# Performance work log

Hardware: AMD Instinct MI355X
Metric: run time of the kernel (lower is better)

## Reference

```python
import jax, jax.numpy as jnp
import numpy as np

B, S, V, D, H, F, GH, NC, L = 64, 256, 50000, 1024, 16, 4096, 100, 7, 4
DH = D // H


def _ln(x, g, b):
    m = x.mean(-1, keepdims=True)
    v = x.var(-1, keepdims=True)
    return (x - m) / jnp.sqrt(v + 1e-5) * g + b


def setup_inputs() -> dict:
    key = jax.random.key(0)
    ks = iter(jax.random.split(key, 40))
    nrm = lambda shp, s=0.02: jax.random.normal(next(ks), shp, jnp.float32) * s
    inp = {}
    inp["src"] = jax.random.randint(next(ks), (B, S), 0, V)
    inp["em_seq"] = jax.random.normal(next(ks), (B, S, 7), jnp.float32)
    inp["d_ids"] = jax.random.randint(next(ks), (B, 1), 0, B)
    inp["ut_len"] = jax.random.randint(next(ks), (B,), 1, S + 1)
    inp["emb"] = jax.random.uniform(next(ks), (V, D), jnp.float32, -0.1, 0.1)
    inp["Wqkv"] = nrm((L, 3 * D, D)); inp["bqkv"] = jnp.zeros((L, 3 * D), jnp.float32)
    inp["Wo"] = nrm((L, D, D)); inp["bo"] = jnp.zeros((L, D), jnp.float32)
    inp["W1"] = nrm((L, F, D)); inp["b1"] = jnp.zeros((L, F), jnp.float32)
    inp["W2"] = nrm((L, D, F)); inp["b2"] = jnp.zeros((L, D), jnp.float32)
    inp["ln1_g"] = jnp.ones((L, D), jnp.float32); inp["ln1_b"] = jnp.zeros((L, D), jnp.float32)
    inp["ln2_g"] = jnp.ones((L, D), jnp.float32); inp["ln2_b"] = jnp.zeros((L, D), jnp.float32)
    inp["gru_Wih"] = nrm((3 * GH, 7), 0.1); inp["gru_Whh"] = nrm((3 * GH, GH), 0.1)
    inp["gru_bih"] = jnp.zeros((3 * GH,), jnp.float32); inp["gru_bhh"] = jnp.zeros((3 * GH,), jnp.float32)
    inp["dec_W"] = jax.random.uniform(next(ks), (NC, 2 * D + GH), jnp.float32, -0.1, 0.1)
    inp["dec_b"] = jnp.zeros((NC,), jnp.float32)
    return inp


def reference(src, em_seq, d_ids, ut_len, emb, Wqkv, bqkv, Wo, bo, W1, b1, W2, b2,
              ln1_g, ln1_b, ln2_g, ln2_b, gru_Wih, gru_Whh, gru_bih, gru_bhh,
              dec_W, dec_b):
    # embedding + scale + sinusoidal positional encoding
    x = emb[src] * jnp.sqrt(jnp.float32(D))                      # [B,S,D]
    pos = jnp.arange(S, dtype=jnp.float32)[:, None]
    div = jnp.exp(jnp.arange(0, D, 2, dtype=jnp.float32) * (-jnp.log(10000.0) / D))
    pe = jnp.stack([jnp.sin(pos * div), jnp.cos(pos * div)], -1).reshape(S, D)
    x = x + pe

    causal = jnp.tril(jnp.ones((S, S), bool))
    neg = jnp.finfo(x.dtype).min
    for l in range(L):  # post-norm transformer encoder layers (PyTorch default)
        qkv = x @ Wqkv[l].T + bqkv[l]
        q, k, v = jnp.split(qkv, 3, -1)
        q = q.reshape(B, S, H, DH); k = k.reshape(B, S, H, DH); v = v.reshape(B, S, H, DH)
        sc = jnp.einsum('bqhd,bkhd->bhqk', q, k) / jnp.sqrt(jnp.float32(DH))
        sc = jnp.where(causal, sc, neg)
        a = jax.nn.softmax(sc, -1)
        o = jnp.einsum('bhqk,bkhd->bqhd', a, v).reshape(B, S, D)
        x = _ln(x + o @ Wo[l].T + bo[l], ln1_g[l], ln1_b[l])
        ff = jax.nn.relu(x @ W1[l].T + b1[l]) @ W2[l].T + b2[l]
        x = _ln(x + ff, ln2_g[l], ln2_b[l])

    # emotion GRU (PyTorch GRU equations), scan over time
    xp = jnp.einsum('bsf,gf->sbg', em_seq, gru_Wih) + gru_bih    # [S,B,3*GH]

    def step(h, xt):
        hp = h @ gru_Whh.T + gru_bhh
        xr, xz, xn = jnp.split(xt, 3, -1)
        hr, hz, hn = jnp.split(hp, 3, -1)
        r = jax.nn.sigmoid(xr + hr)
        z = jax.nn.sigmoid(xz + hz)
        n = jnp.tanh(xn + r * hn)
        h = (1.0 - z) * n + z * h
        return h, h

    _, hs = jax.lax.scan(step, jnp.zeros((B, GH), x.dtype), xp)
    emo = hs.transpose(1, 0, 2)                                  # [B,S,GH]

    # ragged gather of the 'main' utterance per dialogue + broadcast-concat
    lens = ut_len[d_ids[:, 0]]                                   # [B]
    main = x[jnp.arange(B), lens - 1]                            # [B,D]
    pair = jnp.concatenate([x, jnp.broadcast_to(main[:, None, :], (B, S, D))], -1)
    valid = (jnp.arange(S)[None, :] < lens[:, None])[..., None]
    pair = jnp.where(valid, pair, 0.0)                           # zeros beyond ut_len, as in torch loop
    dec_ip = jnp.concatenate([pair, emo], -1)                    # [B,S,2D+GH]
    return dec_ip @ dec_W.T + dec_b                              # [B,S,NC]
```

## Files before the change

kernel.cpp:

```cpp
#include <hip/hip_runtime.h>
#include <hip/hip_bf16.h>
#include <math.h>

#define BB 64
#define SS 256
#define DD 1024
#define HH 16
#define FFN 4096
#define GHH 100
#define NCC 7
#define LL 4
#define TT (BB*SS)
#define DHH 64

typedef unsigned short u16;
typedef unsigned int u32;
typedef __attribute__((ext_vector_type(4))) float f32x4;
typedef __attribute__((ext_vector_type(8))) short s16x8;
typedef __attribute__((ext_vector_type(4))) unsigned short u16x4;

__device__ __forceinline__ u16 f2bf(float f) {
  union { float f; u32 u; } x; x.f = f;
  u32 r = x.u + 0x7FFFu + ((x.u >> 16) & 1u);
  return (u16)(r >> 16);
}
__device__ __forceinline__ float bf2f(u16 b) {
  union { u32 u; float f; } x; x.u = ((u32)b) << 16;
  return x.f;
}

__global__ void k_f2bf4(const float* __restrict__ s0, u16* __restrict__ d0, int n0,
                        const float* __restrict__ s1, u16* __restrict__ d1, int n1,
                        const float* __restrict__ s2, u16* __restrict__ d2, int n2,
                        const float* __restrict__ s3, u16* __restrict__ d3, int n3) {
  int stride = gridDim.x * blockDim.x;
  int total = n0 + n1 + n2 + n3;
  for (int i = blockIdx.x * blockDim.x + threadIdx.x; i < total; i += stride) {
    const float* s; u16* d; int j = i;
    if (j < n0) { s = s0; d = d0; }
    else {
      j -= n0;
      if (j < n1) { s = s1; d = d1; }
      else {
        j -= n1;
        if (j < n2) { s = s2; d = d2; }
        else { j -= n2; s = s3; d = d3; }
      }
    }
    f32x4 v = *(const f32x4*)(s + (size_t)j * 4);
    u16x4 o;
    o[0] = f2bf(v[0]); o[1] = f2bf(v[1]); o[2] = f2bf(v[2]); o[3] = f2bf(v[3]);
    *(u16x4*)(d + (size_t)j * 4) = o;
  }
}

__global__ void k_pe(float* __restrict__ pe) {
  int i = blockIdx.x * blockDim.x + threadIdx.x;
  if (i >= SS * DD / 2) return;
  int s = i / (DD / 2), j = i % (DD / 2);
  float div = __expf((float)(2 * j) * (-9.210340371976184f / (float)DD));
  float a = (float)s * div;
  pe[s * DD + 2 * j]     = sinf(a);
  pe[s * DD + 2 * j + 1] = cosf(a);
}

__global__ void k_embed(const int* __restrict__ src, const float* __restrict__ emb,
                        const float* __restrict__ pe, u16* __restrict__ xb) {
  int i = blockIdx.x * blockDim.x + threadIdx.x;
  if (i >= TT * DD / 4) return;
  int t = i / (DD / 4);
  int d4 = (i % (DD / 4)) * 4;
  int s = t % SS;
  int tok = src[t];
  f32x4 e = *(const f32x4*)(emb + (size_t)tok * DD + d4);
  f32x4 p = *(const f32x4*)(pe + (size_t)s * DD + d4);
  u16x4 o;
  o[0] = f2bf(e[0] * 32.0f + p[0]); o[1] = f2bf(e[1] * 32.0f + p[1]);
  o[2] = f2bf(e[2] * 32.0f + p[2]); o[3] = f2bf(e[3] * 32.0f + p[3]);
  *(u16x4*)(xb + (size_t)t * DD + d4) = o;
}

#define MEMF asm volatile("" ::: "memory")
#define GBAR do { MEMF; __builtin_amdgcn_sched_barrier(0); __builtin_amdgcn_s_barrier(); __builtin_amdgcn_sched_barrier(0); MEMF; } while(0)
#define VMW4 asm volatile("s_waitcnt vmcnt(4)" ::: "memory")

#define STG(P, isB, h, l, buf, kt) \
  __builtin_amdgcn_global_load_lds( \
    (const __attribute__((address_space(1))) u32*)(P[h][l] + (kt)), \
    (__attribute__((address_space(3))) u32*)(smem + (buf)*65536 + (isB)*32768 + (h)*16384 + (l)*8192 + wid*1024), \
    16, 0, 0)

#define LDB(buf) do { \
  _Pragma("unroll") for (int nf = 0; nf < 4; nf++) \
  _Pragma("unroll") for (int kk = 0; kk < 2; kk++) { \
    int rel = (wn*64 + nf*16 + lm)*128 + kk*64 + lg*16; \
    bq[nf][kk] = *(const s16x8*)(smem + (buf)*65536 + 32768 + (rel ^ (((rel>>9)&1)<<5))); \
  } } while(0)

#define LDA(buf, q) do { \
  _Pragma("unroll") for (int ml = 0; ml < 2; ml++) \
  _Pragma("unroll") for (int kk = 0; kk < 2; kk++) { \
    int rel = (wm*128 + ((q)*2+ml)*16 + lm)*128 + kk*64 + lg*16; \
    aq[ml][kk] = *(const s16x8*)(smem + (buf)*65536 + (rel ^ (((rel>>9)&1)<<5))); \
  } } while(0)

#define MFMAQ(q) do { \
  __builtin_amdgcn_s_setprio(1); \
  _Pragma("unroll") for (int ml = 0; ml < 2; ml++) \
  _Pragma("unroll") for (int nf = 0; nf < 4; nf++) \
  _Pragma("unroll") for (int kk = 0; kk < 2; kk++) \
    acc[(q)*2+ml][nf] = __builtin_amdgcn_mfma_f32_16x16x32_bf16(aq[ml][kk], bq[nf][kk], acc[(q)*2+ml][nf], 0, 0, 0); \
  __builtin_amdgcn_s_setprio(0); \
} while(0)

template<int EPI>
__global__ __launch_bounds__(512, 2)
void k_gemm256(const u16* __restrict__ A, const u16* __restrict__ W,
               const float* __restrict__ bias, u16* __restrict__ C,
               int M, int N, int K) {
  extern __shared__ char smem[];
  const int tid = threadIdx.x;
  const int lane = tid & 63;
  const int wid = tid >> 6;
  const int lm = lane & 15, lg = lane >> 4;
  const int wm = wid >> 2, wn = wid & 3;

  const int NB = N >> 8;
  const int nwg = gridDim.x;
  const int bid = blockIdx.x;
  const int cpx = nwg >> 3;
  const int swzb = (bid & 7) * cpx + (bid >> 3);
  const int m0 = (swzb / NB) << 8;
  const int n0 = (swzb % NB) << 8;

  const u16* pA[2][2];
  const u16* pB[2][2];
#pragma unroll
  for (int h = 0; h < 2; h++)
#pragma unroll
    for (int l = 0; l < 2; l++) {
      int rel = h * 16384 + l * 8192 + tid * 16;
      int sb = rel ^ (((rel >> 9) & 1) << 5);
      int grow = sb >> 7;
      int gcol = (sb & 127) >> 1;
      pA[h][l] = A + (size_t)(m0 + grow) * K + gcol;
      pB[h][l] = W + (size_t)(n0 + grow) * K + gcol;
    }

  f32x4 acc[8][4];
#pragma unroll
  for (int i = 0; i < 8; i++)
#pragma unroll
    for (int j = 0; j < 4; j++) acc[i][j] = (f32x4){0.f, 0.f, 0.f, 0.f};

  s16x8 bq[4][2];
  s16x8 aq[2][2];

  const int NT = K >> 6;

  STG(pB,1,0,0,0,0); STG(pB,1,0,1,0,0); STG(pB,1,1,0,0,0); STG(pB,1,1,1,0,0);
  STG(pA,0,0,0,0,0); STG(pA,0,0,1,0,0); STG(pA,0,1,0,0,0); STG(pA,0,1,1,0,0);
  STG(pB,1,0,0,1,64); STG(pB,1,0,1,1,64); STG(pB,1,1,0,1,64); STG(pB,1,1,1,1,64);
  VMW4;
  GBAR;

  for (int i = 0; i < (NT >> 1); i++) {
    const int t1k = (2*i + 1) * 64;
    int t2 = 2*i + 2; if (t2 >= NT) t2 -= NT;
    int t3 = 2*i + 3; if (t3 >= NT) t3 -= NT;
    const int t2k = t2 * 64, t3k = t3 * 64;

    LDB(0); LDA(0,0);
    STG(pA,0,0,0,1,t1k); STG(pA,0,0,1,1,t1k);
    GBAR; MFMAQ(0); GBAR;
    LDA(0,1);
    STG(pA,0,1,0,1,t1k); STG(pA,0,1,1,1,t1k);
    STG(pB,1,0,0,0,t2k); STG(pB,1,0,1,0,t2k);
    GBAR; MFMAQ(1); GBAR;
    LDA(0,2);
    STG(pB,1,1,0,0,t2k); STG(pB,1,1,1,0,t2k);
    GBAR; MFMAQ(2); GBAR;
    LDA(0,3);
    GBAR; MFMAQ(3); VMW4; GBAR;
    LDB(1); LDA(1,0);
    STG(pA,0,0,0,0,t2k); STG(pA,0,0,1,0,t2k);
    GBAR; MFMAQ(0); GBAR;
    LDA(1,1);
    STG(pA,0,1,0,0,t2k); STG(pA,0,1,1,0,t2k);
    GBAR; MFMAQ(1); GBAR;
    LDA(1,2);
    STG(pB,1,0,0,1,t3k); STG(pB,1,0,1,1,t3k);
    GBAR; MFMAQ(2); GBAR;
    LDA(1,3);
    STG(pB,1,1,0,1,t3k); STG(pB,1,1,1,1,t3k);
    GBAR; MFMAQ(3); VMW4; GBAR;
  }

  float bn[4];
#pragma unroll
  for (int nf = 0; nf < 4; nf++) bn[nf] = bias[n0 + wn*64 + nf*16 + lm];
#pragma unroll
  for (int mf = 0; mf < 8; mf++)
#pragma unroll
    for (int nf = 0; nf < 4; nf++) {
      int col = n0 + wn*64 + nf*16 + lm;
#pragma unroll
      for (int r = 0; r < 4; r++) {
        int row = m0 + wm*128 + mf*16 + lg*4 + r;
        float v = acc[mf][nf][r] + bn[nf];
        if (EPI == 1) v = fmaxf(v, 0.f);
        C[(size_t)row * N + col] = f2bf(v);
      }
    }
}

__global__ __launch_bounds__(256, 2)
void k_attn(const u16* __restrict__ qkv, u16* __restrict__ o) {
  const int h = blockIdx.x;
  const int b = blockIdx.y;
  const int lane = threadIdx.x & 63;
  const int w = threadIdx.x >> 6;
  const int lm = lane & 15, lg = lane >> 4;

  __shared__ u16 Ks[64 * 64];
  __shared__ u16 Vt[64 * 64];
  __shared__ u16 Ps[4][64 * 64];

  const size_t tokbase = (size_t)b * SS;

  s16x8 aq[4][2];
#pragma unroll
  for (int mf = 0; mf < 4; mf++) {
    const u16* qrow = qkv + (tokbase + w * 64 + mf * 16 + lm) * 3072 + h * 64;
#pragma unroll
    for (int kk = 0; kk < 2; kk++)
      aq[mf][kk] = *(const s16x8*)(qrow + kk * 32 + lg * 8);
  }

  f32x4 zero = {0.f, 0.f, 0.f, 0.f};
  f32x4 oacc[4][4];
#pragma unroll
  for (int mf = 0; mf < 4; mf++)
#pragma unroll
    for (int df = 0; df < 4; df++) oacc[mf][df] = zero;
  float m_run[16], l_run[16];
#pragma unroll
  for (int r = 0; r < 16; r++) { m_run[r] = -3e38f; l_run[r] = 0.f; }

  for (int kb = 0; kb < 4; kb++) {
    __syncthreads();
    {
      int krow = threadIdx.x >> 2;
      int seg  = (threadIdx.x & 3) * 16;
      const u16* ksrc = qkv + (tokbase + kb * 64 + krow) * 3072 + 1024 + h * 64 + seg;
      s16x8 v0 = *(const s16x8*)(ksrc);
      s16x8 v1 = *(const s16x8*)(ksrc + 8);
      *(s16x8*)&Ks[krow * 64 + seg] = v0;
      *(s16x8*)&Ks[krow * 64 + seg + 8] = v1;
      const u16* vsrc = qkv + (tokbase + kb * 64 + krow) * 3072 + 2048 + h * 64 + seg;
      s16x8 w0 = *(const s16x8*)(vsrc);
      s16x8 w1 = *(const s16x8*)(vsrc + 8);
#pragma unroll
      for (int e = 0; e < 8; e++) {
        Vt[(seg + e) * 64 + krow]     = (u16)w0[e];
        Vt[(seg + 8 + e) * 64 + krow] = (u16)w1[e];
      }
    }
    __syncthreads();
    if (w < kb) continue;

    s16x8 bk[4][2];
#pragma unroll
    for (int nf = 0; nf < 4; nf++)
#pragma unroll
      for (int kk = 0; kk < 2; kk++)
        bk[nf][kk] = *(const s16x8*)&Ks[(nf * 16 + lm) * 64 + kk * 32 + lg * 8];

    const int colbase = kb * 64;
#pragma unroll
    for (int mf = 0; mf < 4; mf++) {
      f32x4 sfr[4];
#pragma unroll
      for (int nf = 0; nf < 4; nf++) {
        f32x4 acc = zero;
#pragma unroll
        for (int kk = 0; kk < 2; kk++)
          acc = __builtin_amdgcn_mfma_f32_16x16x32_bf16(aq[mf][kk], bk[nf][kk], acc, 0, 0, 0);
        sfr[nf] = acc;
      }
      const int rowbase = w * 64 + mf * 16 + lg * 4;
#pragma unroll
      for (int nf = 0; nf < 4; nf++) {
        int col = colbase + nf * 16 + lm;
#pragma unroll
        for (int r = 0; r < 4; r++) {
          float v = sfr[nf][r] * 0.125f;
          sfr[nf][r] = (col <= rowbase + r) ? v : -1e30f;
        }
      }
#pragma unroll
      for (int r = 0; r < 4; r++) {
        float m = fmaxf(fmaxf(sfr[0][r], sfr[1][r]), fmaxf(sfr[2][r], sfr[3][r]));
#pragma unroll
        for (int off = 1; off < 16; off <<= 1) m = fmaxf(m, __shfl_xor(m, off));
        int idx = mf * 4 + r;
        float mnew = fmaxf(m_run[idx], m);
        float fo = __expf(m_run[idx] - mnew);
        m_run[idx] = mnew;
        float ps = 0.f;
#pragma unroll
        for (int nf = 0; nf < 4; nf++) {
          float p = __expf(sfr[nf][r] - mnew);
          sfr[nf][r] = p;
          ps += p;
        }
#pragma unroll
        for (int off = 1; off < 16; off <<= 1) ps += __shfl_xor(ps, off);
        l_run[idx] = l_run[idx] * fo + ps;
#pragma unroll
        for (int df = 0; df < 4; df++) oacc[mf][df][r] *= fo;
      }
#pragma unroll
      for (int nf = 0; nf < 4; nf++)
#pragma unroll
        for (int r = 0; r < 4; r++)
          Ps[w][(mf * 16 + lg * 4 + r) * 64 + nf * 16 + lm] = f2bf(sfr[nf][r]);
    }
    asm volatile("" ::: "memory");
    s16x8 bv[4][2];
#pragma unroll
    for (int df = 0; df < 4; df++)
#pragma unroll
      for (int kk = 0; kk < 2; kk++)
        bv[df][kk] = *(const s16x8*)&Vt[(df * 16 + lm) * 64 + kk * 32 + lg * 8];
#pragma unroll
    for (int mf = 0; mf < 4; mf++) {
      s16x8 pa[2];
#pragma unroll
      for (int kk = 0; kk < 2; kk++)
        pa[kk] = *(const s16x8*)&Ps[w][(mf * 16 + lm) * 64 + kk * 32 + lg * 8];
#pragma unroll
      for (int df = 0; df < 4; df++)
#pragma unroll
        for (int kk = 0; kk < 2; kk++)
          oacc[mf][df] = __builtin_amdgcn_mfma_f32_16x16x32_bf16(pa[kk], bv[df][kk], oacc[mf][df], 0, 0, 0);
    }
  }

#pragma unroll
  for (int mf = 0; mf < 4; mf++)
#pragma unroll
    for (int df = 0; df < 4; df++)
#pragma unroll
      for (int r = 0; r < 4; r++) {
        int row = w * 64 + mf * 16 + lg * 4 + r;
        float val = oacc[mf][df][r] / l_run[mf * 4 + r];
        o[(tokbase + row) * 1024 + h * 64 + df * 16 + lm] = f2bf(val);
      }
}

__global__ __launch_bounds__(256)
void k_ln(u16* __restrict__ xb, const u16* __restrict__ tmp,
          const float* __restrict__ gam, const float* __restrict__ bet) {
  int t = blockIdx.x;
  int tid = threadIdx.x;
  u16x4 a4 = *(const u16x4*)(xb + (size_t)t * DD + tid * 4);
  u16x4 u4 = *(const u16x4*)(tmp + (size_t)t * DD + tid * 4);
  f32x4 v;
#pragma unroll
  for (int e = 0; e < 4; e++) v[e] = bf2f(a4[e]) + bf2f(u4[e]);
  float s = v[0] + v[1] + v[2] + v[3];
  float s2 = v[0]*v[0] + v[1]*v[1] + v[2]*v[2] + v[3]*v[3];
#pragma unroll
  for (int off = 32; off >= 1; off >>= 1) {
    s  += __shfl_xor(s, off);
    s2 += __shfl_xor(s2, off);
  }
  __shared__ float red[8];
  int w = tid >> 6;
  if ((tid & 63) == 0) { red[w] = s; red[4 + w] = s2; }
  __syncthreads();
  s  = red[0] + red[1] + red[2] + red[3];
  s2 = red[4] + red[5] + red[6] + red[7];
  float mean = s * (1.f / 1024.f);
  float var = s2 * (1.f / 1024.f) - mean * mean;
  float rstd = rsqrtf(var + 1e-5f);
  f32x4 g4 = *(const f32x4*)(gam + tid * 4);
  f32x4 b4 = *(const f32x4*)(bet + tid * 4);
  u16x4 yo;
#pragma unroll
  for (int e = 0; e < 4; e++)
    yo[e] = f2bf((v[e] - mean) * rstd * g4[e] + b4[e]);
  *(u16x4*)(xb + (size_t)t * DD + tid * 4) = yo;
}

#define QL(X) X(0) X(1) X(2) X(3) X(4) X(5) X(6) X(7) X(8) X(9) X(10) X(11)
#define F7(X) X(0) X(1) X(2) X(3) X(4) X(5) X(6)

__global__ __launch_bounds__(256, 1)
void k_gru(const float* __restrict__ em, const float* __restrict__ Wih,
           const float* __restrict__ bih, const float* __restrict__ Whh,
           const float* __restrict__ bhh, float* __restrict__ emo) {
  const int b = blockIdx.x;
  const int tid = threadIdx.x;
  const int iraw = tid >> 1;
  const int i = iraw < 100 ? iraw : 99;
  const bool act = iraw < 100;
  const int half = tid & 1;
  __shared__ __align__(16) float h[2][104];

  const float* rowR = Whh + (size_t)i * 100 + half * 50;
  const float* rowZ = Whh + (size_t)(100 + i) * 100 + half * 50;
  const float* rowN = Whh + (size_t)(200 + i) * 100 + half * 50;

#define LOADQ(q) \
  f32x4 wr##q = {rowR[4*q], rowR[4*q+1], rowR[4*q+2], rowR[4*q+3]}; \
  f32x4 wz##q = {rowZ[4*q], rowZ[4*q+1], rowZ[4*q+2], rowZ[4*q+3]}; \
  f32x4 wn##q = {rowN[4*q], rowN[4*q+1], rowN[4*q+2], rowN[4*q+3]};
  QL(LOADQ)
#undef LOADQ
  f32x4 wr12 = {rowR[48], rowR[49], 0.f, 0.f};
  f32x4 wz12 = {rowZ[48], rowZ[49], 0.f, 0.f};
  f32x4 wn12 = {rowN[48], rowN[49], 0.f, 0.f};

#define LOADI(f) \
  float wir##f = Wih[i * 7 + f]; \
  float wiz##f = Wih[(100 + i) * 7 + f]; \
  float win##f = Wih[(200 + i) * 7 + f];
  F7(LOADI)
#undef LOADI
  const float br = bhh[i], bz = bhh[100 + i], bn = bhh[200 + i];
  const float xbr = bih[i], xbz = bih[100 + i], xbn = bih[200 + i];

  if (tid < 104) { h[0][tid] = 0.f; h[1][tid] = 0.f; }
  __syncthreads();

  const float* eb = em + (size_t)b * SS * 7;
#define DECLE(f) float e##f = eb[f];
  F7(DECLE)
#undef DECLE

  for (int s = 0; s < SS; ++s) {
    const int cur = s & 1, nxt = cur ^ 1;
    float sr = xbr, sz = xbz, sn = xbn;
#define MACI(f) sr += wir##f * e##f; sz += wiz##f * e##f; sn += win##f * e##f;
    F7(MACI)
#undef MACI
    {
      int sp = (s + 1 < SS) ? s + 1 : s;
#define LDE(f) e##f = eb[sp * 7 + f];
      F7(LDE)
#undef LDE
    }
    const float* hb = &h[cur][half * 52];
    f32x4 ar4 = {0.f,0.f,0.f,0.f}, az4 = {0.f,0.f,0.f,0.f}, an4 = {0.f,0.f,0.f,0.f};
#define MACQ(q) { f32x4 hv = *(const f32x4*)(hb + 4*q); \
    ar4 += wr##q * hv; az4 += wz##q * hv; an4 += wn##q * hv; }
    QL(MACQ) MACQ(12)
#undef MACQ
    float ar = (ar4[0] + ar4[1]) + (ar4[2] + ar4[3]);
    float az = (az4[0] + az4[1]) + (az4[2] + az4[3]);
    float an = (an4[0] + an4[1]) + (an4[2] + an4[3]);
    ar += __shfl_xor(ar, 1);
    az += __shfl_xor(az, 1);
    an += __shfl_xor(an, 1);
    if (act && half == 0) {
      int slot = i + (i >= 50 ? 2 : 0);
      float hold = h[cur][slot];
      float rr = 1.f / (1.f + __expf(-(sr + ar + br)));
      float zz = 1.f / (1.f + __expf(-(sz + az + bz)));
      float nx = sn + rr * (an + bn);
      float e2 = __expf(-2.f * fabsf(nx));
      float th = (1.f - e2) / (1.f + e2);
      float nn = copysignf(th, nx);
      float hn = (1.f - zz) * nn + zz * hold;
      h[nxt][slot] = hn;
      emo[((size_t)b * SS + s) * GHH + i] = hn;
    }
    __syncthreads();
  }
}

__global__ void k_main(const int* __restrict__ d_ids, const int* __restrict__ ut_len,
                       const u16* __restrict__ x, const float* __restrict__ decW,
                       float* __restrict__ md) {
  int b = blockIdx.x;
  int lane = threadIdx.x;
  int len = ut_len[d_ids[b]];
  const u16* xr = x + ((size_t)b * SS + (len - 1)) * DD;
  float acc[NCC];
#pragma unroll
  for (int c = 0; c < NCC; c++) acc[c] = 0.f;
  for (int d = lane; d < DD; d += 64) {
    float xv = bf2f(xr[d]);
#pragma unroll
    for (int c = 0; c < NCC; c++) acc[c] += xv * decW[(size_t)c * 2148 + 1024 + d];
  }
#pragma unroll
  for (int c = 0; c < NCC; c++) {
#pragma unroll
    for (int off = 32; off >= 1; off >>= 1) acc[c] += __shfl_xor(acc[c], off);
  }
  if (lane == 0) {
#pragma unroll
    for (int c = 0; c < NCC; c++) md[b * NCC + c] = acc[c];
  }
}

__global__ __launch_bounds__(256)
void k_dec(const u16* __restrict__ x, const float* __restrict__ emo,
           const float* __restrict__ md, const float* __restrict__ decW,
           const float* __restrict__ decb, const int* __restrict__ d_ids,
           const int* __restrict__ ut_len, float* __restrict__ out) {
  int grp = threadIdx.x >> 6, lane = threadIdx.x & 63;
  int t = blockIdx.x * 4 + grp;
  int b = t / SS, s = t % SS;
  int len = ut_len[d_ids[b]];
  bool valid = s < len;
  float acc[NCC];
#pragma unroll
  for (int c = 0; c < NCC; c++) acc[c] = 0.f;
  if (valid) {
    const u16* xrow = x + (size_t)t * DD;
    for (int d = lane; d < DD; d += 64) {
      float xv = bf2f(xrow[d]);
#pragma unroll
      for (int c = 0; c < NCC; c++) acc[c] += xv * decW[(size_t)c * 2148 + d];
    }
  }
  {
    const float* er = emo + (size_t)t * GHH;
    for (int d = lane; d < GHH; d += 64) {
      float ev = er[d];
#pragma unroll
      for (int c = 0; c < NCC; c++) acc[c] += ev * decW[(size_t)c * 2148 + 2048 + d];
    }
  }
#pragma unroll
  for (int c = 0; c < NCC; c++) {
#pragma unroll
    for (int off = 32; off >= 1; off >>= 1) acc[c] += __shfl_xor(acc[c], off);
  }
  if (lane == 0) {
#pragma unroll
    for (int c = 0; c < NCC; c++) {
      float v = acc[c] + (valid ? md[b * NCC + c] : 0.f) + decb[c];
      out[(size_t)t * NCC + c] = v;
    }
  }
}

extern "C" void kernel_launch(void* const* d_in, const int* in_sizes, int n_in,
                              void* d_out, int out_size, void* d_ws, size_t ws_size,
                              hipStream_t stream) {
  const int*   src    = (const int*)d_in[0];
  const float* em_seq = (const float*)d_in[1];
  const int*   d_ids  = (const int*)d_in[2];
  const int*   ut_len = (const int*)d_in[3];
  const float* emb    = (const float*)d_in[4];
  const float* Wqkv   = (const float*)d_in[5];
  const float* bqkv   = (const float*)d_in[6];
  const float* Wo     = (const float*)d_in[7];
  const float* bo     = (const float*)d_in[8];
  const float* W1     = (const float*)d_in[9];
  const float* b1     = (const float*)d_in[10];
  const float* W2     = (const float*)d_in[11];
  const float* b2     = (const float*)d_in[12];
  const float* ln1g   = (const float*)d_in[13];
  const float* ln1b   = (const float*)d_in[14];
  const float* ln2g   = (const float*)d_in[15];
  const float* ln2b   = (const float*)d_in[16];
  const float* gWih   = (const float*)d_in[17];
  const float* gWhh   = (const float*)d_in[18];
  const float* gbih   = (const float*)d_in[19];
  const float* gbhh   = (const float*)d_in[20];
  const float* decW   = (const float*)d_in[21];
  const float* decb   = (const float*)d_in[22];
  float* out = (float*)d_out;

  char* wsp = (char*)d_ws;
  auto take = [&](size_t n) { char* p = wsp; wsp += (n + 255) & ~(size_t)255; return p; };

  u16*   wqkvb = (u16*)take((size_t)3072 * 1024 * 2);
  u16*   wob   = (u16*)take((size_t)1024 * 1024 * 2);
  u16*   w1b   = (u16*)take((size_t)4096 * 1024 * 2);
  u16*   w2b   = (u16*)take((size_t)1024 * 4096 * 2);
  float* pe    = (float*)take((size_t)SS * DD * 4);
  u16*   xb    = (u16*)take((size_t)TT * DD * 2);
  u16*   big   = (u16*)take((size_t)TT * FFN * 2);
  u16*   ob    = (u16*)take((size_t)TT * DD * 2);
  u16*   tmp16 = (u16*)take((size_t)TT * DD * 2);
  float* emo   = (float*)take((size_t)BB * SS * GHH * 4);
  float* md    = (float*)take((size_t)BB * NCC * 4);

  (void)hipFuncSetAttribute((const void*)&k_gemm256<0>,
      hipFuncAttributeMaxDynamicSharedMemorySize, 131072);
  (void)hipFuncSetAttribute((const void*)&k_gemm256<1>,
      hipFuncAttributeMaxDynamicSharedMemorySize, 131072);

  k_gru<<<BB, 256, 0, stream>>>(em_seq, gWih, gbih, gWhh, gbhh, emo);

  k_pe<<<(SS * DD / 2 + 255) / 256, 256, 0, stream>>>(pe);
  k_embed<<<TT * DD / 4 / 256, 256, 0, stream>>>(src, emb, pe, xb);

  for (int l = 0; l < LL; ++l) {
    k_f2bf4<<<2048, 256, 0, stream>>>(
        Wqkv + (size_t)l * 3072 * 1024, wqkvb, 3072 * 1024 / 4,
        Wo   + (size_t)l * 1024 * 1024, wob,   1024 * 1024 / 4,
        W1   + (size_t)l * 4096 * 1024, w1b,   4096 * 1024 / 4,
        W2   + (size_t)l * 1024 * 4096, w2b,   1024 * 4096 / 4);

    k_gemm256<0><<<(TT/256) * (3072/256), 512, 131072, stream>>>(
        xb, wqkvb, bqkv + (size_t)l * 3072, big, TT, 3072, 1024);
    k_attn<<<dim3(HH, BB), 256, 0, stream>>>(big, ob);
    k_gemm256<0><<<(TT/256) * (1024/256), 512, 131072, stream>>>(
        ob, wob, bo + (size_t)l * 1024, tmp16, TT, 1024, 1024);
    k_ln<<<TT, 256, 0, stream>>>(xb, tmp16, ln1g + (size_t)l * DD, ln1b + (size_t)l * DD);
    k_gemm256<1><<<(TT/256) * (4096/256), 512, 131072, stream>>>(
        xb, w1b, b1 + (size_t)l * 4096, big, TT, 4096, 1024);
    k_gemm256<0><<<(TT/256) * (1024/256), 512, 131072, stream>>>(
        big, w2b, b2 + (size_t)l * 1024, tmp16, TT, 1024, 4096);
    k_ln<<<TT, 256, 0, stream>>>(xb, tmp16, ln2g + (size_t)l * DD, ln2b + (size_t)l * DD);
  }

  k_main<<<BB, 64, 0, stream>>>(d_ids, ut_len, xb, decW, md);
  k_dec<<<TT / 4, 256, 0, stream>>>(xb, emo, md, decW, decb, d_ids, ut_len, out);
}
```

Measured before the change: 2.324 ms.

## Split GRU gates across threads with shared-memory gate combine

Restructures the GRU recurrence kernel so each hidden unit's three gate rows are handled by separate thread pairs (6 threads per unit, 640 threads per block) instead of one pair computing all three gates. Partial gate sums are written to shared memory, and after an extra barrier the first 100 threads apply the nonlinearities and update h. This cuts the per-thread serial FMA chain and register use on the sequential critical path, at the cost of an additional __syncthreads per timestep. The GRU is a small part of the total runtime, dominated by the transformer GEMMs, unless it sits on the critical path.

```diff
diff --git a/kernel.cpp b/kernel.cpp
--- a/kernel.cpp
+++ b/kernel.cpp
@@ -394,88 +394,84 @@
   *(u16x4*)(xb + (size_t)t * DD + tid * 4) = yo;
 }
 
-#define QL(X) X(0) X(1) X(2) X(3) X(4) X(5) X(6) X(7) X(8) X(9) X(10) X(11)
 #define F7(X) X(0) X(1) X(2) X(3) X(4) X(5) X(6)
-
-__global__ __launch_bounds__(256, 1)
+#define Q12(X) X(0) X(1) X(2) X(3) X(4) X(5) X(6) X(7) X(8) X(9) X(10) X(11)
+
+__global__ __launch_bounds__(640, 1)
 void k_gru(const float* __restrict__ em, const float* __restrict__ Wih,
            const float* __restrict__ bih, const float* __restrict__ Whh,
            const float* __restrict__ bhh, float* __restrict__ emo) {
   const int b = blockIdx.x;
   const int tid = threadIdx.x;
-  const int iraw = tid >> 1;
-  const int i = iraw < 100 ? iraw : 99;
+  const int iraw = tid / 6;
+  const int sub = tid - iraw * 6;
+  const int g = sub >> 1, half = sub & 1;
   const bool act = iraw < 100;
-  const int half = tid & 1;
+  const int i = act ? iraw : 99;
+  const int grow = g * 100 + i;
+
   __shared__ __align__(16) float h[2][104];
-
-  const float* rowR = Whh + (size_t)i * 100 + half * 50;
-  const float* rowZ = Whh + (size_t)(100 + i) * 100 + half * 50;
-  const float* rowN = Whh + (size_t)(200 + i) * 100 + half * 50;
-
-#define LOADQ(q) \
-  f32x4 wr##q = {rowR[4*q], rowR[4*q+1], rowR[4*q+2], rowR[4*q+3]}; \
-  f32x4 wz##q = {rowZ[4*q], rowZ[4*q+1], rowZ[4*q+2], rowZ[4*q+3]}; \
-  f32x4 wn##q = {rowN[4*q], rowN[4*q+1], rowN[4*q+2], rowN[4*q+3]};
-  QL(LOADQ)
-#undef LOADQ
-  f32x4 wr12 = {rowR[48], rowR[49], 0.f, 0.f};
-  f32x4 wz12 = {rowZ[48], rowZ[49], 0.f, 0.f};
-  f32x4 wn12 = {rowN[48], rowN[49], 0.f, 0.f};
-
-#define LOADI(f) \
-  float wir##f = Wih[i * 7 + f]; \
-  float wiz##f = Wih[(100 + i) * 7 + f]; \
-  float win##f = Wih[(200 + i) * 7 + f];
-  F7(LOADI)
-#undef LOADI
-  const float br = bhh[i], bz = bhh[100 + i], bn = bhh[200 + i];
-  const float xbr = bih[i], xbz = bih[100 + i], xbn = bih[200 + i];
+  __shared__ float vals[400];
+
+  const float* rowP = Whh + (size_t)grow * 100 + half * 50;
+#define LQ(q) f32x4 w##q = {rowP[4*(q)], rowP[4*(q)+1], rowP[4*(q)+2], rowP[4*(q)+3]}; \
+  asm volatile("" : "+v"(w##q));
+  Q12(LQ)
+#undef LQ
+  f32x4 w12 = {rowP[48], rowP[49], 0.f, 0.f};
+  asm volatile("" : "+v"(w12));
+
+#define LI(f) float wi##f = Wih[grow * 7 + (f)];
+  F7(LI)
+#undef LI
+  const float bhhv = bhh[grow];
+  const float bihv = bih[grow];
 
   if (tid < 104) { h[0][tid] = 0.f; h[1][tid] = 0.f; }
   __syncthreads();
 
   const float* eb = em + (size_t)b * SS * 7;
-#define DECLE(f) float e##f = eb[f];
-  F7(DECLE)
-#undef DECLE
+#define DE(f) float e##f = eb[f];
+  F7(DE)
+#undef DE
 
   for (int s = 0; s < SS; ++s) {
-    const int cur = s & 1, nxt = cur ^ 1;
-    float sr = xbr, sz = xbz, sn = xbn;
-#define MACI(f) sr += wir##f * e##f; sz += wiz##f * e##f; sn += win##f * e##f;
-    F7(MACI)
-#undef MACI
+    const float* hc = h[s & 1];
+    float* hb_next = h[(s & 1) ^ 1];
+    float xp = bihv;
+#define MI(f) xp += wi##f * e##f;
+    F7(MI)
+#undef MI
     {
       int sp = (s + 1 < SS) ? s + 1 : s;
-#define LDE(f) e##f = eb[sp * 7 + f];
-      F7(LDE)
-#undef LDE
-    }
-    const float* hb = &h[cur][half * 52];
-    f32x4 ar4 = {0.f,0.f,0.f,0.f}, az4 = {0.f,0.f,0.f,0.f}, an4 = {0.f,0.f,0.f,0.f};
-#define MACQ(q) { f32x4 hv = *(const f32x4*)(hb + 4*q); \
-    ar4 += wr##q * hv; az4 += wz##q * hv; an4 += wn##q * hv; }
-    QL(MACQ) MACQ(12)
-#undef MACQ
-    float ar = (ar4[0] + ar4[1]) + (ar4[2] + ar4[3]);
-    float az = (az4[0] + az4[1]) + (az4[2] + az4[3]);
-    float an = (an4[0] + an4[1]) + (an4[2] + an4[3]);
-    ar += __shfl_xor(ar, 1);
-    az += __shfl_xor(az, 1);
-    an += __shfl_xor(an, 1);
+#define LE(f) e##f = eb[sp * 7 + (f)];
+      F7(LE)
+#undef LE
+    }
+    const float* hbp = hc + half * 52;
+    f32x4 a4 = {0.f, 0.f, 0.f, 0.f};
+#define MQ(q) { f32x4 hv = *(const f32x4*)(hbp + 4*(q)); a4 += w##q * hv; }
+    Q12(MQ) MQ(12)
+#undef MQ
+    float a = (a4[0] + a4[1]) + (a4[2] + a4[3]);
+    a += __shfl_xor(a, 1);
     if (act && half == 0) {
-      int slot = i + (i >= 50 ? 2 : 0);
-      float hold = h[cur][slot];
-      float rr = 1.f / (1.f + __expf(-(sr + ar + br)));
-      float zz = 1.f / (1.f + __expf(-(sz + az + bz)));
-      float nx = sn + rr * (an + bn);
+      if (g == 2) { vals[200 + i] = xp; vals[300 + i] = a + bhhv; }
+      else        { vals[g * 100 + i] = xp + a + bhhv; }
+    }
+    __syncthreads();
+    if (tid < 100) {
+      int slot = tid + (tid >= 50 ? 2 : 0);
+      float hold = hc[slot];
+      float rr = 1.f / (1.f + __expf(-vals[tid]));
+      float zz = 1.f / (1.f + __expf(-vals[100 + tid]));
+      float nx = vals[200 + tid] + rr * vals[300 + tid];
       float e2 = __expf(-2.f * fabsf(nx));
       float th = (1.f - e2) / (1.f + e2);
       float nn = copysignf(th, nx);
-      float hn = (1.f - zz) * nn + zz * hold;
-      h[nxt][slot] = hn;
-      emo[((size_t)b * SS + s) * GHH + i] = hn;
+      float hv = (1.f - zz) * nn + zz * hold;
+      hb_next[slot] = hv;
+      emo[((size_t)b * SS + s) * GHH + tid] = hv;
     }
     __syncthreads();
   }
@@ -598,7 +594,7 @@
   (void)hipFuncSetAttribute((const void*)&k_gemm256<1>,
       hipFuncAttributeMaxDynamicSharedMemorySize, 131072);
 
-  k_gru<<<BB, 256, 0, stream>>>(em_seq, gWih, gbih, gWhh, gbhh, emo);
+  k_gru<<<BB, 640, 0, stream>>>(em_seq, gWih, gbih, gWhh, gbhh, emo);
 
   k_pe<<<(SS * DD / 2 + 255) / 256, 256, 0, stream>>>(pe);
   k_embed<<<TT * DD / 4 / 256, 256, 0, stream>>>(src, emb, pe, xb);
```

Result: no change. 2.347 ms (+1.0%).
